# Kernel optimization log

Measured on AMD Instinct MI355X. Metric: run time of the kernel, lower is better.

## Reference

```python
import jax, jax.numpy as jnp
import numpy as np

N, C, L, NUM_LAYERS = 512, 32, 1024, 3
BN_EPS = 1e-5


def setup_inputs() -> dict:
    key = jax.random.key(0)
    kx, kw, kb, kg, kbe = jax.random.split(key, 5)
    x = jax.random.normal(kx, (N, C, L), dtype=jnp.float32)
    # Per-channel, per-layer Linear weights: (C, num_layers, L_out, L_in)
    W = jax.random.normal(kw, (C, NUM_LAYERS, L, L), dtype=jnp.float32) / np.float32(np.sqrt(L))
    b = 0.01 * jax.random.normal(kb, (C, NUM_LAYERS, L), dtype=jnp.float32)
    # BatchNorm affine params for the num_layers-1 inner BN layers
    gamma = 1.0 + 0.1 * jax.random.normal(kg, (C, NUM_LAYERS - 1, L), dtype=jnp.float32)
    beta = 0.1 * jax.random.normal(kbe, (C, NUM_LAYERS - 1, L), dtype=jnp.float32)
    return {"x": x, "W": W, "b": b, "gamma": gamma, "beta": beta}


def reference(x, W, b, gamma, beta):
    """Fused per-channel MLP head.

    x: (N, C, L). For each channel c, applies num_layers Linear layers with
    ReLU + BatchNorm1d (training-mode batch stats, biased variance) between
    layers. All C channels computed as one batched GEMM per layer.
    """
    h = x
    for i in range(NUM_LAYERS):
        # batched per-channel Linear: (N,C,Lin) x (C,Lout,Lin) -> (N,C,Lout)
        h = jnp.einsum('ncl,cml->ncm', h, W[:, i]) + b[:, i][None]
        if i < NUM_LAYERS - 1:
            h = jax.nn.relu(h)
            # BatchNorm1d over the batch dim N, per (channel, feature)
            mean = jnp.mean(h, axis=0)          # (C, L)
            var = jnp.var(h, axis=0)            # biased variance, matches torch BN
            h = (h - mean) * jax.lax.rsqrt(var + BN_EPS) * gamma[:, i] + beta[:, i]
    return h
```

## Files before the change

### kernel.cpp

```cpp
#include <hip/hip_runtime.h>
#include <hip/hip_bf16.h>

#define NB 512
#define CCH 32
#define LF 1024
#define CL (CCH * LF)
#define BN_EPS 1e-5f

typedef __bf16 bf16x8 __attribute__((ext_vector_type(8)));
typedef __bf16 bf16x4 __attribute__((ext_vector_type(4)));
typedef float f32x4 __attribute__((ext_vector_type(4)));

#define QSTRIDE 1032

template <bool BNA, bool RELU>
__global__ __launch_bounds__(256, 2) void gemm_k(
    const float* __restrict__ Abase, const float* __restrict__ Wall,
    const float* __restrict__ ball, const float* __restrict__ scale,
    const float* __restrict__ shift, float* __restrict__ Out, int layer) {
  __shared__ __bf16 As[4 * QSTRIDE];
  __shared__ __bf16 Bs[4 * QSTRIDE];

  const int tid = threadIdx.x;
  const int c = blockIdx.y;
  const int mtile = blockIdx.x & 3;
  const int ntile = blockIdx.x >> 2;

  const float* A = Abase + c * LF;
  const float* Wp = Wall + (size_t)(c * 3 + layer) * LF * LF;
  const float* bias = ball + (c * 3 + layer) * LF;
  const float* scl = BNA ? scale + c * LF : nullptr;
  const float* shf = BNA ? shift + c * LF : nullptr;

  const int lane = tid & 63;
  const int wv = tid >> 6;
  const int wm = (wv & 1) * 64;
  const int wn = (wv >> 1) * 64;
  const int l15 = lane & 15;
  const int quad = lane >> 4;

  const int sr = tid >> 3;
  const int kseg = tid & 7;
  const int q = kseg >> 1;
  const int bsub = (kseg & 1) * 4;

  f32x4 acc[4][4] = {};

  for (int kt = 0; kt < LF / 32; ++kt) {
    const int k0 = kt * 32 + kseg * 4;

    f32x4 sc, sh;
    if (BNA) {
      sc = *(const f32x4*)(scl + k0);
      sh = *(const f32x4*)(shf + k0);
    }
#pragma unroll
    for (int i = 0; i < 4; ++i) {
      const int r = i * 32 + sr;
      f32x4 v = *(const f32x4*)(A + (size_t)(mtile * 128 + r) * CL + k0);
      if (BNA) v = v * sc + sh;
      bf16x4 o = {(__bf16)v.x, (__bf16)v.y, (__bf16)v.z, (__bf16)v.w};
      *(bf16x4*)&As[q * QSTRIDE + r * 8 + bsub] = o;
    }
#pragma unroll
    for (int i = 0; i < 4; ++i) {
      const int r = i * 32 + sr;
      f32x4 v = *(const f32x4*)(Wp + (size_t)(ntile * 128 + r) * LF + k0);
      bf16x4 o = {(__bf16)v.x, (__bf16)v.y, (__bf16)v.z, (__bf16)v.w};
      *(bf16x4*)&Bs[q * QSTRIDE + r * 8 + bsub] = o;
    }
    __syncthreads();

    bf16x8 af[4], bfr[4];
#pragma unroll
    for (int mi = 0; mi < 4; ++mi)
      af[mi] = *(const bf16x8*)&As[quad * QSTRIDE + (wm + mi * 16 + l15) * 8];
#pragma unroll
    for (int ni = 0; ni < 4; ++ni)
      bfr[ni] = *(const bf16x8*)&Bs[quad * QSTRIDE + (wn + ni * 16 + l15) * 8];
#pragma unroll
    for (int mi = 0; mi < 4; ++mi)
#pragma unroll
      for (int ni = 0; ni < 4; ++ni)
        acc[mi][ni] = __builtin_amdgcn_mfma_f32_16x16x32_bf16(
            af[mi], bfr[ni], acc[mi][ni], 0, 0, 0);
    __syncthreads();
  }

  float* outp = Out + (size_t)c * LF;
#pragma unroll
  for (int ni = 0; ni < 4; ++ni) {
    const int feat = ntile * 128 + wn + ni * 16 + l15;
    const float bv = bias[feat];
#pragma unroll
    for (int mi = 0; mi < 4; ++mi) {
      const int row0 = mtile * 128 + wm + mi * 16 + quad * 4;
#pragma unroll
      for (int r = 0; r < 4; ++r) {
        float v = acc[mi][ni][r] + bv;
        if (RELU) v = fmaxf(v, 0.f);
        outp[(size_t)(row0 + r) * CL + feat] = v;
      }
    }
  }
}

__global__ __launch_bounds__(256) void bn_stats(
    const float* __restrict__ H, const float* __restrict__ gamma,
    const float* __restrict__ beta, float* __restrict__ scale,
    float* __restrict__ shift, int bnlayer) {
  __shared__ float s_sum[256], s_sq[256];
  const int tid = threadIdx.x;
  const int f = tid & 63, g = tid >> 6;
  const int c = blockIdx.y;
  const int l = blockIdx.x * 64 + f;
  const float* col = H + (size_t)c * LF + l;
  float sum = 0.f, sq = 0.f;
  for (int n = g; n < NB; n += 4) {
    float v = col[(size_t)n * CL];
    sum += v;
    sq += v * v;
  }
  s_sum[tid] = sum;
  s_sq[tid] = sq;
  __syncthreads();
  if (g == 0) {
    sum = s_sum[f] + s_sum[64 + f] + s_sum[128 + f] + s_sum[192 + f];
    sq = s_sq[f] + s_sq[64 + f] + s_sq[128 + f] + s_sq[192 + f];
    const float mean = sum * (1.f / NB);
    const float var = sq * (1.f / NB) - mean * mean;
    const float rstd = rsqrtf(var + BN_EPS);
    const float ga = gamma[(size_t)(c * 2 + bnlayer) * LF + l];
    const float be = beta[(size_t)(c * 2 + bnlayer) * LF + l];
    const float sc = rstd * ga;
    scale[(size_t)c * LF + l] = sc;
    shift[(size_t)c * LF + l] = be - mean * sc;
  }
}

extern "C" void kernel_launch(void* const* d_in, const int* in_sizes, int n_in,
                              void* d_out, int out_size, void* d_ws,
                              size_t ws_size, hipStream_t stream) {
  const float* x = (const float*)d_in[0];
  const float* W = (const float*)d_in[1];
  const float* b = (const float*)d_in[2];
  const float* gamma = (const float*)d_in[3];
  const float* beta = (const float*)d_in[4];
  float* out = (float*)d_out;

  float* scale0 = (float*)d_ws;
  float* shift0 = scale0 + CCH * LF;
  float* scale1 = shift0 + CCH * LF;
  float* shift1 = scale1 + CCH * LF;
  float* h2 = shift1 + CCH * LF;

  const dim3 blk(256);
  const dim3 ggrid(32, 32);
  const dim3 sgrid(16, 32);

  gemm_k<false, true><<<ggrid, blk, 0, stream>>>(x, W, b, nullptr, nullptr, out, 0);
  bn_stats<<<sgrid, blk, 0, stream>>>(out, gamma, beta, scale0, shift0, 0);
  gemm_k<true, true><<<ggrid, blk, 0, stream>>>(out, W, b, scale0, shift0, h2, 1);
  bn_stats<<<sgrid, blk, 0, stream>>>(h2, gamma, beta, scale1, shift1, 1);
  gemm_k<true, false><<<ggrid, blk, 0, stream>>>(h2, W, b, scale1, shift1, out, 2);
}
```

Measured before the change: 941.7 us.

## Fold BatchNorm into bf16 weights, pre-convert activations, use direct-to-LDS loads

```diff
diff --git a/kernel.cpp b/kernel.cpp
--- a/kernel.cpp
+++ b/kernel.cpp
@@ -11,26 +11,85 @@
 typedef __bf16 bf16x4 __attribute__((ext_vector_type(4)));
 typedef float f32x4 __attribute__((ext_vector_type(4)));
 
-#define QSTRIDE 1032
-
-template <bool BNA, bool RELU>
+__device__ __forceinline__ void gload16(const void* g, void* l) {
+  auto gp = (const __attribute__((address_space(1))) void*)(uintptr_t)g;
+  auto lp = (__attribute__((address_space(3))) void*)(uint32_t)(uintptr_t)l;
+  __builtin_amdgcn_global_load_lds(gp, lp, 16, 0, 0);
+}
+
+__global__ __launch_bounds__(256) void cvt_x(const float* __restrict__ x,
+                                             __bf16* __restrict__ xb) {
+  const int c = blockIdx.y;
+  const int wv = threadIdx.x >> 6, lane = threadIdx.x & 63;
+  const int n0 = blockIdx.x * 8;
+#pragma unroll
+  for (int rr = 0; rr < 2; ++rr) {
+    const int n = n0 + wv * 2 + rr;
+    const float* src = x + ((size_t)n * CCH + c) * LF;
+    __bf16* dst = xb + ((size_t)c * NB + n) * LF;
+#pragma unroll
+    for (int j = 0; j < 4; ++j) {
+      const int col = (j * 64 + lane) * 4;
+      f32x4 v = *(const f32x4*)(src + col);
+      bf16x4 o = {(__bf16)v.x, (__bf16)v.y, (__bf16)v.z, (__bf16)v.w};
+      *(bf16x4*)(dst + col) = o;
+    }
+  }
+}
+
+template <bool HAS_BN>
+__global__ __launch_bounds__(256) void fold_w(
+    const float* __restrict__ Wall, const float* __restrict__ ball,
+    const float* __restrict__ scale, const float* __restrict__ shift,
+    __bf16* __restrict__ Wb, float* __restrict__ bout, int layer) {
+  const int c = blockIdx.y;
+  const int wv = threadIdx.x >> 6, lane = threadIdx.x & 63;
+  const float* Wp = Wall + (size_t)(c * 3 + layer) * LF * LF;
+  const float* scl = scale + (size_t)c * LF;
+  const float* shf = shift + (size_t)c * LF;
+  const int m0 = blockIdx.x * 16 + wv * 4;
+#pragma unroll
+  for (int rr = 0; rr < 4; ++rr) {
+    const int m = m0 + rr;
+    const float* wrow = Wp + (size_t)m * LF;
+    __bf16* orow = Wb + (size_t)c * LF * LF + (size_t)m * LF;
+    float dot = 0.f;
+#pragma unroll
+    for (int j = 0; j < 4; ++j) {
+      const int col = (j * 64 + lane) * 4;
+      f32x4 w = *(const f32x4*)(wrow + col);
+      if (HAS_BN) {
+        f32x4 s = *(const f32x4*)(scl + col);
+        f32x4 t = *(const f32x4*)(shf + col);
+        dot += w.x * t.x + w.y * t.y + w.z * t.z + w.w * t.w;
+        f32x4 wsc = w * s;
+        bf16x4 o = {(__bf16)wsc.x, (__bf16)wsc.y, (__bf16)wsc.z, (__bf16)wsc.w};
+        *(bf16x4*)(orow + col) = o;
+      } else {
+        bf16x4 o = {(__bf16)w.x, (__bf16)w.y, (__bf16)w.z, (__bf16)w.w};
+        *(bf16x4*)(orow + col) = o;
+      }
+    }
+    if (HAS_BN) {
+#pragma unroll
+      for (int off = 32; off >= 1; off >>= 1) dot += __shfl_down(dot, off);
+    }
+    if (lane == 0)
+      bout[(size_t)c * LF + m] =
+          ball[(size_t)(c * 3 + layer) * LF + m] + (HAS_BN ? dot : 0.f);
+  }
+}
+
+template <bool RELU, bool OUTBF>
 __global__ __launch_bounds__(256, 2) void gemm_k(
-    const float* __restrict__ Abase, const float* __restrict__ Wall,
-    const float* __restrict__ ball, const float* __restrict__ scale,
-    const float* __restrict__ shift, float* __restrict__ Out, int layer) {
-  __shared__ __bf16 As[4 * QSTRIDE];
-  __shared__ __bf16 Bs[4 * QSTRIDE];
-
+    const __bf16* __restrict__ Ab, const __bf16* __restrict__ Wb,
+    const float* __restrict__ bf, void* __restrict__ Out) {
+  __shared__ __bf16 As[128 * 32];
+  __shared__ __bf16 Bs[128 * 32];
   const int tid = threadIdx.x;
   const int c = blockIdx.y;
   const int mtile = blockIdx.x & 3;
   const int ntile = blockIdx.x >> 2;
-
-  const float* A = Abase + c * LF;
-  const float* Wp = Wall + (size_t)(c * 3 + layer) * LF * LF;
-  const float* bias = ball + (c * 3 + layer) * LF;
-  const float* scl = BNA ? scale + c * LF : nullptr;
-  const float* shf = BNA ? shift + c * LF : nullptr;
 
   const int lane = tid & 63;
   const int wv = tid >> 6;
@@ -39,45 +98,33 @@
   const int l15 = lane & 15;
   const int quad = lane >> 4;
 
-  const int sr = tid >> 3;
-  const int kseg = tid & 7;
-  const int q = kseg >> 1;
-  const int bsub = (kseg & 1) * 4;
+  const int srow = lane >> 2;
+  const int skel = (lane & 3) * 8;
+
+  const __bf16* Ag = Ab + (size_t)c * NB * LF +
+                     (size_t)(mtile * 128 + wv * 32 + srow) * LF + skel;
+  const __bf16* Bg = Wb + (size_t)c * LF * LF +
+                     (size_t)(ntile * 128 + wv * 32 + srow) * LF + skel;
+  __bf16* Al = &As[(wv * 32) * 32];
+  __bf16* Bl = &Bs[(wv * 32) * 32];
 
   f32x4 acc[4][4] = {};
 
   for (int kt = 0; kt < LF / 32; ++kt) {
-    const int k0 = kt * 32 + kseg * 4;
-
-    f32x4 sc, sh;
-    if (BNA) {
-      sc = *(const f32x4*)(scl + k0);
-      sh = *(const f32x4*)(shf + k0);
-    }
-#pragma unroll
-    for (int i = 0; i < 4; ++i) {
-      const int r = i * 32 + sr;
-      f32x4 v = *(const f32x4*)(A + (size_t)(mtile * 128 + r) * CL + k0);
-      if (BNA) v = v * sc + sh;
-      bf16x4 o = {(__bf16)v.x, (__bf16)v.y, (__bf16)v.z, (__bf16)v.w};
-      *(bf16x4*)&As[q * QSTRIDE + r * 8 + bsub] = o;
-    }
-#pragma unroll
-    for (int i = 0; i < 4; ++i) {
-      const int r = i * 32 + sr;
-      f32x4 v = *(const f32x4*)(Wp + (size_t)(ntile * 128 + r) * LF + k0);
-      bf16x4 o = {(__bf16)v.x, (__bf16)v.y, (__bf16)v.z, (__bf16)v.w};
-      *(bf16x4*)&Bs[q * QSTRIDE + r * 8 + bsub] = o;
-    }
+    const int k0 = kt * 32;
+    gload16(Ag + k0, Al);
+    gload16(Ag + 16 * LF + k0, Al + 16 * 32);
+    gload16(Bg + k0, Bl);
+    gload16(Bg + 16 * LF + k0, Bl + 16 * 32);
     __syncthreads();
 
     bf16x8 af[4], bfr[4];
 #pragma unroll
     for (int mi = 0; mi < 4; ++mi)
-      af[mi] = *(const bf16x8*)&As[quad * QSTRIDE + (wm + mi * 16 + l15) * 8];
+      af[mi] = *(const bf16x8*)&As[(wm + mi * 16 + l15) * 32 + quad * 8];
 #pragma unroll
     for (int ni = 0; ni < 4; ++ni)
-      bfr[ni] = *(const bf16x8*)&Bs[quad * QSTRIDE + (wn + ni * 16 + l15) * 8];
+      bfr[ni] = *(const bf16x8*)&Bs[(wn + ni * 16 + l15) * 32 + quad * 8];
 #pragma unroll
     for (int mi = 0; mi < 4; ++mi)
 #pragma unroll
@@ -87,26 +134,46 @@
     __syncthreads();
   }
 
-  float* outp = Out + (size_t)c * LF;
-#pragma unroll
-  for (int ni = 0; ni < 4; ++ni) {
-    const int feat = ntile * 128 + wn + ni * 16 + l15;
-    const float bv = bias[feat];
-#pragma unroll
-    for (int mi = 0; mi < 4; ++mi) {
-      const int row0 = mtile * 128 + wm + mi * 16 + quad * 4;
-#pragma unroll
-      for (int r = 0; r < 4; ++r) {
-        float v = acc[mi][ni][r] + bv;
-        if (RELU) v = fmaxf(v, 0.f);
-        outp[(size_t)(row0 + r) * CL + feat] = v;
+  const float* bias = bf + (size_t)c * LF;
+  if (OUTBF) {
+    __bf16* outp = (__bf16*)Out + (size_t)c * NB * LF;
+#pragma unroll
+    for (int ni = 0; ni < 4; ++ni) {
+      const int feat = ntile * 128 + wn + ni * 16 + l15;
+      const float bvv = bias[feat];
+#pragma unroll
+      for (int mi = 0; mi < 4; ++mi) {
+        const int row0 = mtile * 128 + wm + mi * 16 + quad * 4;
+#pragma unroll
+        for (int r = 0; r < 4; ++r) {
+          float v = acc[mi][ni][r] + bvv;
+          if (RELU) v = fmaxf(v, 0.f);
+          outp[(size_t)(row0 + r) * LF + feat] = (__bf16)v;
+        }
       }
     }
+  } else {
+    float* outp = (float*)Out + (size_t)c * LF;
+#pragma unroll
+    for (int ni = 0; ni < 4; ++ni) {
+      const int feat = ntile * 128 + wn + ni * 16 + l15;
+      const float bvv = bias[feat];
+#pragma unroll
+      for (int mi = 0; mi < 4; ++mi) {
+        const int row0 = mtile * 128 + wm + mi * 16 + quad * 4;
+#pragma unroll
+        for (int r = 0; r < 4; ++r) {
+          float v = acc[mi][ni][r] + bvv;
+          if (RELU) v = fmaxf(v, 0.f);
+          outp[(size_t)(row0 + r) * CL + feat] = v;
+        }
+      }
+    }
   }
 }
 
 __global__ __launch_bounds__(256) void bn_stats(
-    const float* __restrict__ H, const float* __restrict__ gamma,
+    const __bf16* __restrict__ H, const float* __restrict__ gamma,
     const float* __restrict__ beta, float* __restrict__ scale,
     float* __restrict__ shift, int bnlayer) {
   __shared__ float s_sum[256], s_sq[256];
@@ -114,10 +181,10 @@
   const int f = tid & 63, g = tid >> 6;
   const int c = blockIdx.y;
   const int l = blockIdx.x * 64 + f;
-  const float* col = H + (size_t)c * LF + l;
+  const __bf16* col = H + (size_t)c * NB * LF + l;
   float sum = 0.f, sq = 0.f;
   for (int n = g; n < NB; n += 4) {
-    float v = col[(size_t)n * CL];
+    float v = (float)col[(size_t)n * LF];
     sum += v;
     sq += v * v;
   }
@@ -148,19 +215,27 @@
   const float* beta = (const float*)d_in[4];
   float* out = (float*)d_out;
 
-  float* scale0 = (float*)d_ws;
-  float* shift0 = scale0 + CCH * LF;
-  float* scale1 = shift0 + CCH * LF;
-  float* shift1 = scale1 + CCH * LF;
-  float* h2 = shift1 + CCH * LF;
+  char* ws = (char*)d_ws;
+  float* scale = (float*)ws;  ws += (size_t)CL * 4;
+  float* shift = (float*)ws;  ws += (size_t)CL * 4;
+  float* bfold = (float*)ws;  ws += (size_t)CL * 4;
+  __bf16* xb = (__bf16*)ws;   ws += (size_t)NB * CL * 2;
+  __bf16* h1 = (__bf16*)ws;   ws += (size_t)NB * CL * 2;
+  __bf16* h2 = (__bf16*)ws;   ws += (size_t)NB * CL * 2;
+  __bf16* Wfold = (__bf16*)ws;
 
   const dim3 blk(256);
   const dim3 ggrid(32, 32);
+  const dim3 fgrid(64, 32);
   const dim3 sgrid(16, 32);
 
-  gemm_k<false, true><<<ggrid, blk, 0, stream>>>(x, W, b, nullptr, nullptr, out, 0);
-  bn_stats<<<sgrid, blk, 0, stream>>>(out, gamma, beta, scale0, shift0, 0);
-  gemm_k<true, true><<<ggrid, blk, 0, stream>>>(out, W, b, scale0, shift0, h2, 1);
-  bn_stats<<<sgrid, blk, 0, stream>>>(h2, gamma, beta, scale1, shift1, 1);
-  gemm_k<true, false><<<ggrid, blk, 0, stream>>>(h2, W, b, scale1, shift1, out, 2);
-}
+  cvt_x<<<fgrid, blk, 0, stream>>>(x, xb);
+  fold_w<false><<<fgrid, blk, 0, stream>>>(W, b, scale, shift, Wfold, bfold, 0);
+  gemm_k<true, true><<<ggrid, blk, 0, stream>>>(xb, Wfold, bfold, h1);
+  bn_stats<<<sgrid, blk, 0, stream>>>(h1, gamma, beta, scale, shift, 0);
+  fold_w<true><<<fgrid, blk, 0, stream>>>(W, b, scale, shift, Wfold, bfold, 1);
+  gemm_k<true, true><<<ggrid, blk, 0, stream>>>(h1, Wfold, bfold, h2);
+  bn_stats<<<sgrid, blk, 0, stream>>>(h2, gamma, beta, scale, shift, 1);
+  fold_w<true><<<fgrid, blk, 0, stream>>>(W, b, scale, shift, Wfold, bfold, 2);
+  gemm_k<false, false><<<ggrid, blk, 0, stream>>>(h2, Wfold, bfold, out);
+}
```

After: 867.0 us. -7.9%, faster.
